# Optimization experiments

Measured on AMD Instinct MI355X. Metric: run time of the kernel, lower is better.

Reference implementation:

```python
import jax, jax.numpy as jnp
import numpy as np

SR = 22050
FL = 1024      # window_samples
FP = 256       # step_samples
FCEIL = 10000  # formant ceiling (Hz)
MAXF = 4       # max formants
AP_ORDER = 10
R_ORDER = 30
FMIN, FMAX = 50, 500
DK_ITERS = 60  # Durand-Kerner iterations (replaces companion-matrix eig; differentiable)

_w = np.blackman(FL)
WIN = jnp.asarray(_w / np.sqrt(np.sum(_w ** 2)), jnp.float32)  # power-normalized blackman (diffsptk default)


def _frame(x):
    # center-padded framing, frames = T//FP + 1
    pad = FL // 2
    xp = jnp.pad(x, ((0, 0), (pad, pad)))
    n_frames = x.shape[-1] // FP + 1
    idx = jnp.arange(n_frames)[:, None] * FP + jnp.arange(FL)[None, :]
    return xp[:, idx]  # [B, F, FL]


def _levinson(r, order):
    # Levinson-Durbin on autocorrelation r[..., :order+1].
    # Returns (allpole poly coeffs a[..., order+1] with a0=1, reflection coeffs k[..., order]).
    a = jnp.zeros(r.shape[:-1] + (order + 1,), r.dtype).at[..., 0].set(1.0)
    E = r[..., 0]
    ks = []
    for m in range(1, order + 1):
        if m == 1:
            acc = r[..., 1]
        else:
            acc = r[..., m] + jnp.sum(a[..., 1:m] * r[..., m - 1:0:-1], axis=-1)
        k = -acc / (E + 1e-9)
        a_prev = a
        a = a.at[..., m].set(k)
        if m > 1:
            a = a.at[..., 1:m].add(k[..., None] * a_prev[..., m - 1:0:-1])
        E = E * (1.0 - k * k)
        ks.append(k)
    return a, jnp.stack(ks, axis=-1)


def _poly_roots(coeffs):
    # Durand-Kerner simultaneous root iteration, vectorized over frames.
    n = coeffs.shape[-1] - 1
    c = (coeffs / coeffs[..., :1]).astype(jnp.complex64)
    z0 = (0.4 + 0.9j) ** jnp.arange(1, n + 1)
    z = jnp.broadcast_to(z0, c.shape[:-1] + (n,)).astype(jnp.complex64)
    eye = jnp.eye(n, dtype=jnp.complex64)
    def step(z, _):
        p = jnp.zeros_like(z)
        for i in range(n + 1):  # Horner eval of poly at all current root estimates
            p = p * z + c[..., i:i + 1]
        diff = z[..., :, None] - z[..., None, :] + eye
        z = z - p / (jnp.prod(diff, axis=-1) + 1e-12)
        return z, None
    z, _ = jax.lax.scan(step, z, None, length=DK_ITERS)
    return z  # [..., n]


def _root_to_formant(roots):
    # downsampled spectrum covers 0..FCEIL/2, so freq = angle/(2*pi)*FCEIL
    ang = jnp.angle(roots)
    freq = ang / (2.0 * jnp.pi) * FCEIL
    freq = jnp.where(ang > 1e-4, freq, FCEIL * 0.5)  # keep upper-half-plane roots only
    return jnp.sort(freq, axis=-1)[..., :MAXF]  # [B, F, MAXF]


def _pitch(x):
    # autocorrelation pitch tracker
    xf = _frame(x)
    spec = jnp.fft.rfft(xf)
    ac = jnp.fft.irfft(spec * jnp.conj(spec))
    lag_min, lag_max = SR // FMAX, SR // FMIN  # 44..441
    seg = ac[..., lag_min:lag_max + 1]
    peak = jnp.max(seg, axis=-1)
    idx = jnp.argmax(seg, axis=-1)
    nccf = peak / (ac[..., 0] + 1e-9)
    pitch = SR / (lag_min + idx).astype(jnp.float32)
    voicing = (nccf > 0.3).astype(jnp.float32)
    return pitch, voicing, nccf


def _forward(x):
    xf = _frame(x)                 # [B, F, FL]
    xw = xf * WIN
    spec = jnp.fft.rfft(xw)        # [B, F, 513]
    nb = spec.shape[-1]
    ds = int(FCEIL / SR * nb)      # 232 bins -> Nyquist FCEIL/2
    x_ds = spec[..., :ds]
    ac_ds = jnp.fft.irfft(x_ds * jnp.conj(x_ds))   # [B, F, 462]
    ac_us = jnp.fft.irfft(spec * jnp.conj(spec))   # [B, F, 1024]
    ap_env, _ = _levinson(ac_ds, AP_ORDER)
    _, r_coeff_ref = _levinson(ac_us, R_ORDER)
    roots = _poly_roots(ap_env)
    formants = _root_to_formant(roots)
    energy = 10.0 * jnp.log10(jnp.sum(xf * xf, axis=-1) + 1e-10)
    mag = jnp.abs(jnp.fft.rfft(xf))
    freqs = jnp.arange(nb, dtype=jnp.float32) * (SR / FL)
    centroid = jnp.sum(mag * freqs, axis=-1) / (jnp.sum(mag, axis=-1) + 1e-10)
    tilt = ac_ds[..., 1] / (ac_ds[..., 0] + 1e-10)
    pitch, voicing, nccf = _pitch(x)
    pitch = jnp.log(pitch)
    return (formants, energy, centroid, tilt, pitch, voicing, r_coeff_ref, x_ds, nccf)


def setup_inputs() -> dict:
    key = jax.random.key(0)
    x = jax.random.normal(key, (8, 661500), jnp.float32)
    return {"x": x}


def reference(x):
    return _forward(x)
```

## Files before the change

### kernel.cpp

```cpp
#include <hip/hip_runtime.h>
#include <math.h>

#define NSAMP   661500
#define NFRAME  2584
#define NFTOT   20672

#define EN_OFF    82688
#define CEN_OFF   103360
#define TILT_OFF  124032
#define PITCH_OFF 144704
#define VOI_OFF   165376
#define RC_OFF    186048
#define XDS_OFF   806208

__device__ __forceinline__ float waveReduceSum(float v) {
  #pragma unroll
  for (int m = 1; m < 64; m <<= 1) v += __shfl_xor(v, m, 64);
  return v;
}

__device__ __forceinline__ float blockReduceSum(float v, float* s) {
  v = waveReduceSum(v);
  const int w = threadIdx.x >> 6;
  if ((threadIdx.x & 63) == 0) s[w] = v;
  __syncthreads();
  v = s[0] + s[1] + s[2] + s[3];
  __syncthreads();
  return v;
}

__device__ __forceinline__ void blockReduceSum2(float& v0, float& v1, float* s) {
  v0 = waveReduceSum(v0);
  v1 = waveReduceSum(v1);
  const int w = threadIdx.x >> 6;
  if ((threadIdx.x & 63) == 0) { s[w] = v0; s[4 + w] = v1; }
  __syncthreads();
  v0 = s[0] + s[1] + s[2] + s[3];
  v1 = s[4] + s[5] + s[6] + s[7];
  __syncthreads();
}

__device__ __forceinline__ void fft1024p(float2* X, float2* Y, const float2* tw, int tid) {
  int m = 1;
  #pragma unroll
  for (int s = 0; s < 5; ++s) {
    const int k  = tid & (m - 1);
    const int jm = tid - k;
    const float2 a0 = X[tid];
    const float2 a1 = X[tid + 256];
    const float2 a2 = X[tid + 512];
    const float2 a3 = X[tid + 768];
    const float2 w1 = tw[jm];
    float2 sA, dA, sB, dB;
    sA.x = a0.x + a2.x; sA.y = a0.y + a2.y;
    { const float dx = a0.x - a2.x, dy = a0.y - a2.y;
      dA.x = dx * w1.x + dy * w1.y;
      dA.y = dy * w1.x - dx * w1.y; }
    sB.x = a1.x + a3.x; sB.y = a1.y + a3.y;
    { const float dx = a1.x - a3.x, dy = a1.y - a3.y;
      const float wx = -w1.y, wy = w1.x;
      dB.x = dx * wx + dy * wy;
      dB.y = dy * wx - dx * wy; }
    const float w2x = w1.x * w1.x - w1.y * w1.y;
    const float w2y = 2.0f * w1.x * w1.y;
    const int B = 4 * tid - 3 * k;
    { float2 o;
      o.x = sA.x + sB.x; o.y = sA.y + sB.y;
      Y[B] = o;
      const float dx = sA.x - sB.x, dy = sA.y - sB.y;
      o.x = dx * w2x + dy * w2y;
      o.y = dy * w2x - dx * w2y;
      Y[B + 2 * m] = o; }
    { float2 o;
      o.x = dA.x + dB.x; o.y = dA.y + dB.y;
      Y[B + m] = o;
      const float dx = dA.x - dB.x, dy = dA.y - dB.y;
      o.x = dx * w2x + dy * w2y;
      o.y = dy * w2x - dx * w2y;
      Y[B + 3 * m] = o; }
    __syncthreads();
    float2* tmp = X; X = Y; Y = tmp;
    m <<= 2;
  }
}

template<int ORDER>
__device__ __forceinline__ void levinson_d(const double* r, double* a) {
  double E = r[0];
  a[0] = 1.0;
  #pragma unroll
  for (int m = 1; m <= ORDER; ++m) {
    double acc = r[m];
    #pragma unroll
    for (int i = 1; i < m; ++i) acc += a[i] * r[m - i];
    const double kk = -acc / (E + 1e-9);
    #pragma unroll
    for (int i = 1; i <= (m - 1) / 2; ++i) {
      const double t1 = a[i], t2 = a[m - i];
      a[i]     = t1 + kk * t2;
      a[m - i] = t2 + kk * t1;
    }
    if ((m & 1) == 0) { const double t = a[m >> 1]; a[m >> 1] = t + kk * t; }
    a[m] = kk;
    E *= (1.0 - kk * kk);
  }
}

__device__ __forceinline__ void levinson_f30(const float* r, float* gk) {
  float a[31];
  float E = r[0];
  a[0] = 1.0f;
  #pragma unroll
  for (int m = 1; m <= 30; ++m) {
    float acc = r[m];
    #pragma unroll
    for (int i = 1; i < m; ++i) acc += a[i] * r[m - i];
    const float kk = -acc / (E + 1e-9f);
    #pragma unroll
    for (int i = 1; i <= (m - 1) / 2; ++i) {
      const float t1 = a[i], t2 = a[m - i];
      a[i]     = t1 + kk * t2;
      a[m - i] = t2 + kk * t1;
    }
    if ((m & 1) == 0) { const float t = a[m >> 1]; a[m >> 1] = t + kk * t; }
    a[m] = kk;
    E *= (1.0f - kk * kk);
    if (gk) gk[m - 1] = kk;
  }
}

__global__ void __launch_bounds__(256, 6)
feat_mono4(const float* __restrict__ x, float* __restrict__ out,
           const int xds_pf, const int nccf_off) {
  __shared__ float2 A[1024];
  __shared__ float2 Bb[1024];
  __shared__ float2 tw[256];
  __shared__ float  Pw[232];
  __shared__ float  sred[8];
  __shared__ int    sredi[4];
  __shared__ float  stash[4][42];
  __shared__ float  aprt[4][11];

  const int tid   = threadIdx.x;
  const int w     = tid >> 6;
  const int lane  = tid & 63;
  const int fbase = blockIdx.x * 4;

  {
    const float th = (float)tid * (6.2831853071795864769f / 1024.0f);
    float sn, cn;
    sincosf(th, &sn, &cn);
    tw[tid] = make_float2(cn, sn);
  }
  float wv[4];
  float wsq = 0.0f;
  #pragma unroll
  for (int q = 0; q < 4; ++q) {
    const int n = tid + q * 256;
    const float th = (float)n * (6.2831853071795864769f / 1023.0f);
    const float wn = 0.42f - 0.5f * cosf(th) + 0.08f * cosf(2.0f * th);
    wv[q] = wn;
    wsq += wn * wn;
  }
  float ctab[11];
  #pragma unroll
  for (int l = 0; l < 11; ++l)
    ctab[l] = cosf((float)(tid * l) * (6.2831853071795864769f / 462.0f));
  const float wgt462 = ((tid == 0 || tid == 231) ? 1.0f : 2.0f) * (1.0f / 462.0f);
  __syncthreads();
  const float invn = 1.0f / sqrtf(blockReduceSum(wsq, sred));

  #pragma unroll 1
  for (int p = 0; p < 4; ++p) {
    const int fg = fbase + p;
    const int bb = fg / NFRAME;
    const int fr = fg - bb * NFRAME;
    const float* xb = x + (size_t)bb * NSAMP;

    float esum = 0.0f;
    #pragma unroll
    for (int q = 0; q < 4; ++q) {
      const int n = tid + q * 256;
      const int g = fr * 256 + n - 512;
      const float xv = (g >= 0 && g < NSAMP) ? xb[g] : 0.0f;
      esum += xv * xv;
      A[n] = make_float2(xv * wv[q] * invn, xv);
    }
    esum = waveReduceSum(esum);
    if (lane == 0) sred[w] = esum;
    __syncthreads();
    if (tid == 0) {
      const float en = sred[0] + sred[1] + sred[2] + sred[3];
      out[EN_OFF + fg] = 10.0f * log10f(en + 1e-10f);
    }

    fft1024p(A, Bb, tw, tid);

    float cs0 = 0.0f, cs1 = 0.0f;
    for (int k = tid; k < 513; k += 256) {
      const float2 Zk = Bb[k];
      const float2 Zn = Bb[(1024 - k) & 1023];
      const float xwr = 0.5f * (Zk.x + Zn.x);
      const float xwi = 0.5f * (Zk.y - Zn.y);
      const float xfr = 0.5f * (Zk.y + Zn.y);
      const float xfi = -0.5f * (Zk.x - Zn.x);
      const float pw = xwr * xwr + xwi * xwi;
      const float pf = xfr * xfr + xfi * xfi;
      const float mg = sqrtf(pf);
      cs0 += mg;
      cs1 += mg * ((float)k * (22050.0f / 1024.0f));
      if (k < 232) {
        Pw[k] = pw;
        if (xds_pf == 232) {
          out[XDS_OFF + (size_t)fg * 232 + k] = xwr;
        } else {
          out[XDS_OFF + (size_t)fg * 464 + 2 * k]     = xwr;
          out[XDS_OFF + (size_t)fg * 464 + 2 * k + 1] = xwi;
        }
      }
    }
    blockReduceSum2(cs0, cs1, sred);
    if (tid == 0) out[CEN_OFF + fg] = cs1 / (cs0 + 1e-10f);

    #pragma unroll
    for (int q = 0; q < 4; ++q) {
      const int k2 = tid + q * 256;
      const int km = (k2 <= 512) ? k2 : (1024 - k2);
      const float2 Zk = Bb[km];
      const float2 Zn = Bb[(1024 - km) & 1023];
      const float xwr = 0.5f * (Zk.x + Zn.x);
      const float xwi = 0.5f * (Zk.y - Zn.y);
      const float xfr = 0.5f * (Zk.y + Zn.y);
      const float xfi = -0.5f * (Zk.x - Zn.x);
      const float pw = xwr * xwr + xwi * xwi;
      const float pf = xfr * xfr + xfi * xfi;
      A[k2] = make_float2(pw * 1024.0f, pf);
    }
    __syncthreads();

    fft1024p(A, Bb, tw, tid);

    float pv = -3.0e38f;
    int   pl = 1 << 30;
    for (int l = 44 + tid; l <= 441; l += 256) {
      const float v = Bb[l].y;
      if (v > pv) { pv = v; pl = l; }
    }
    #pragma unroll
    for (int m = 1; m < 64; m <<= 1) {
      const float ov = __shfl_xor(pv, m, 64);
      const int   ol = __shfl_xor(pl, m, 64);
      if (ov > pv || (ov == pv && ol < pl)) { pv = ov; pl = ol; }
    }
    if (lane == 0) { sred[w] = pv; sredi[w] = pl; }
    __syncthreads();
    if (tid == 0) {
      float bv = sred[0]; int bl = sredi[0];
      #pragma unroll
      for (int q = 1; q < 4; ++q)
        if (sred[q] > bv || (sred[q] == bv && sredi[q] < bl)) { bv = sred[q]; bl = sredi[q]; }
      const float ac0  = Bb[0].y * (1.0f / 1024.0f);
      const float peak = bv * (1.0f / 1024.0f);
      const float nccf = peak / (ac0 + 1e-9f);
      out[PITCH_OFF + fg] = logf(22050.0f / (float)bl);
      out[VOI_OFF + fg]   = (nccf > 0.3f) ? 1.0f : 0.0f;
      out[nccf_off + fg]  = nccf;
    }

    const float pwW = (tid < 232) ? Pw[tid] * wgt462 : 0.0f;
    #pragma unroll
    for (int l = 0; l < 11; ++l) {
      const float t = waveReduceSum(pwW * ctab[l]);
      if (lane == 0) aprt[w][l] = t;
    }
    __syncthreads();
    if (tid < 11)
      stash[p][31 + tid] = aprt[0][tid] + aprt[1][tid] + aprt[2][tid] + aprt[3][tid];
    if (tid == 0) {
      const float a0 = aprt[0][0] + aprt[1][0] + aprt[2][0] + aprt[3][0];
      const float a1 = aprt[0][1] + aprt[1][1] + aprt[2][1] + aprt[3][1];
      out[TILT_OFF + fg] = a1 / (a0 + 1e-10f);
    }
    if (tid < 31) stash[p][tid] = Bb[tid].x * (1.0f / 1048576.0f);
    __syncthreads();
  }

  if (w == 0) {
    const int g     = lane >> 4;
    const int ri    = lane & 15;
    const int gbase = g << 4;
    const int fg    = fbase + g;

    levinson_f30(&stash[g][0],
                 (ri == 0) ? (out + RC_OFF + (size_t)fg * 30) : (float*)nullptr);

    double rds[11], a10[11];
    #pragma unroll
    for (int l = 0; l < 11; ++l) rds[l] = (double)stash[g][31 + l];
    levinson_d<10>(rds, a10);

    double zr = 0.4, zi = 0.9;
    for (int q = 0; q < ri; ++q) {
      const double nr = zr * 0.4 - zi * 0.9;
      zi = zr * 0.9 + zi * 0.4;
      zr = nr;
    }
    for (int it = 0; it < 60; ++it) {
      double pr = 1.0, pi = 0.0;
      #pragma unroll
      for (int q = 1; q <= 10; ++q) {
        const double nr = pr * zr - pi * zi + a10[q];
        pi = pr * zi + pi * zr;
        pr = nr;
      }
      double dr = 1.0, di = 0.0;
      #pragma unroll
      for (int j = 0; j < 10; ++j) {
        const double ozr = __shfl(zr, gbase + j, 64);
        const double ozi = __shfl(zi, gbase + j, 64);
        const double er = (j == ri) ? 1.0 : (zr - ozr);
        const double ei = (j == ri) ? 0.0 : (zi - ozi);
        const double nr = dr * er - di * ei;
        di = dr * ei + di * er;
        dr = nr;
      }
      dr += 1e-12;
      const double d2 = dr * dr + di * di;
      const double qr = (pr * dr + pi * di) / d2;
      const double qi = (pi * dr - pr * di) / d2;
      zr -= qr;
      zi -= qi;
    }
    const double ang = atan2(zi, zr);
    double freq = (ang > 0.0001) ? (ang / 6.283185307179586476925287 * 10000.0) : 5000.0;
    if (ri >= 10) freq = 1.0e300;
    double fsel[4];
    #pragma unroll
    for (int p2 = 0; p2 < 4; ++p2) {
      double mn = freq;
      #pragma unroll
      for (int m = 1; m < 16; m <<= 1) mn = fmin(mn, __shfl_xor(mn, m, 64));
      fsel[p2] = mn;
      const unsigned long long bal =
          __ballot(freq == mn) & (0xFFFFULL << gbase);
      const int low = (int)__builtin_ctzll(bal);
      if (lane == low) freq = 1.0e300;
    }
    if (ri == 0) {
      out[(size_t)fg * 4 + 0] = (float)fsel[0];
      out[(size_t)fg * 4 + 1] = (float)fsel[1];
      out[(size_t)fg * 4 + 2] = (float)fsel[2];
      out[(size_t)fg * 4 + 3] = (float)fsel[3];
    }
  }
}

extern "C" void kernel_launch(void* const* d_in, const int* in_sizes, int n_in,
                              void* d_out, int out_size, void* d_ws, size_t ws_size,
                              hipStream_t stream) {
  (void)in_sizes; (void)n_in; (void)d_ws; (void)ws_size;
  const float* x = (const float*)d_in[0];
  float* out = (float*)d_out;
  int xds_pf = 232;
  if (out_size >= XDS_OFF + NFTOT * 464 + NFTOT) xds_pf = 464;
  const int nccf_off = XDS_OFF + NFTOT * xds_pf;
  feat_mono4<<<dim3(NFTOT / 4), dim3(256), 0, stream>>>(x, out, xds_pf, nccf_off);
}
```

Before: 379.1 us.

## Process six frames per block and pack root-finding lanes ten per frame

Each block now handles six frames instead of four, and the wave-0 Durand-Kerner stage packs ten lanes per frame instead of sixteen, so 60 of 64 lanes do useful work. This cuts the per-block setup cost (twiddles, window, cos table) and the serial root-finding tail relative to the frame work. The formant top-4 selection becomes a per-lane sort over shuffled values rather than ballot-based reductions, and the complex division uses one reciprocal. Launch bounds are raised to 7 blocks per SM, which may force register spilling. The last block handles a partial tile, which adds guard logic.

```diff
diff --git a/kernel.cpp b/kernel.cpp
--- a/kernel.cpp
+++ b/kernel.cpp
@@ -4,6 +4,8 @@
 #define NSAMP   661500
 #define NFRAME  2584
 #define NFTOT   20672
+#define FPB     6
+#define NBLK    3446
 
 #define EN_OFF    82688
 #define CEN_OFF   103360
@@ -129,8 +131,8 @@
   }
 }
 
-__global__ void __launch_bounds__(256, 6)
-feat_mono4(const float* __restrict__ x, float* __restrict__ out,
+__global__ void __launch_bounds__(256, 7)
+feat_mono6(const float* __restrict__ x, float* __restrict__ out,
            const int xds_pf, const int nccf_off) {
   __shared__ float2 A[1024];
   __shared__ float2 Bb[1024];
@@ -138,13 +140,14 @@
   __shared__ float  Pw[232];
   __shared__ float  sred[8];
   __shared__ int    sredi[4];
-  __shared__ float  stash[4][42];
+  __shared__ float  stash[FPB][42];
   __shared__ float  aprt[4][11];
 
   const int tid   = threadIdx.x;
   const int w     = tid >> 6;
   const int lane  = tid & 63;
-  const int fbase = blockIdx.x * 4;
+  const int fbase = blockIdx.x * FPB;
+  const int np    = (fbase + FPB <= NFTOT) ? FPB : (NFTOT - fbase);
 
   {
     const float th = (float)tid * (6.2831853071795864769f / 1024.0f);
@@ -171,7 +174,7 @@
   const float invn = 1.0f / sqrtf(blockReduceSum(wsq, sred));
 
   #pragma unroll 1
-  for (int p = 0; p < 4; ++p) {
+  for (int p = 0; p < np; ++p) {
     const int fg = fbase + p;
     const int bb = fg / NFRAME;
     const int fr = fg - bb * NFRAME;
@@ -286,17 +289,19 @@
   }
 
   if (w == 0) {
-    const int g     = lane >> 4;
-    const int ri    = lane & 15;
-    const int gbase = g << 4;
-    const int fg    = fbase + g;
-
-    levinson_f30(&stash[g][0],
-                 (ri == 0) ? (out + RC_OFF + (size_t)fg * 30) : (float*)nullptr);
+    const int g     = lane / 10;
+    const int ri    = lane - g * 10;
+    const int gbase = g * 10;
+    const int gg    = (g < FPB) ? g : (FPB - 1);
+    const bool act  = (g < np);
+    const int fg    = fbase + gg;
+
+    levinson_f30(&stash[gg][0],
+                 (ri == 0 && act) ? (out + RC_OFF + (size_t)fg * 30) : (float*)nullptr);
 
     double rds[11], a10[11];
     #pragma unroll
-    for (int l = 0; l < 11; ++l) rds[l] = (double)stash[g][31 + l];
+    for (int l = 0; l < 11; ++l) rds[l] = (double)stash[gg][31 + l];
     levinson_d<10>(rds, a10);
 
     double zr = 0.4, zi = 0.9;
@@ -325,32 +330,38 @@
         dr = nr;
       }
       dr += 1e-12;
-      const double d2 = dr * dr + di * di;
-      const double qr = (pr * dr + pi * di) / d2;
-      const double qi = (pi * dr - pr * di) / d2;
+      const double inv = 1.0 / (dr * dr + di * di);
+      const double qr = (pr * dr + pi * di) * inv;
+      const double qi = (pi * dr - pr * di) * inv;
       zr -= qr;
       zi -= qi;
     }
     const double ang = atan2(zi, zr);
     double freq = (ang > 0.0001) ? (ang / 6.283185307179586476925287 * 10000.0) : 5000.0;
     if (ri >= 10) freq = 1.0e300;
-    double fsel[4];
+
+    double f[10];
+    #pragma unroll
+    for (int j = 0; j < 10; ++j) f[j] = __shfl(freq, gbase + j, 64);
+    bool used[10];
+    #pragma unroll
+    for (int j = 0; j < 10; ++j) used[j] = false;
+    float o4[4];
     #pragma unroll
     for (int p2 = 0; p2 < 4; ++p2) {
-      double mn = freq;
+      double mn = 1.0e300;
+      int mj = -1;
       #pragma unroll
-      for (int m = 1; m < 16; m <<= 1) mn = fmin(mn, __shfl_xor(mn, m, 64));
-      fsel[p2] = mn;
-      const unsigned long long bal =
-          __ballot(freq == mn) & (0xFFFFULL << gbase);
-      const int low = (int)__builtin_ctzll(bal);
-      if (lane == low) freq = 1.0e300;
-    }
-    if (ri == 0) {
-      out[(size_t)fg * 4 + 0] = (float)fsel[0];
-      out[(size_t)fg * 4 + 1] = (float)fsel[1];
-      out[(size_t)fg * 4 + 2] = (float)fsel[2];
-      out[(size_t)fg * 4 + 3] = (float)fsel[3];
+      for (int j = 0; j < 10; ++j)
+        if (!used[j] && f[j] < mn) { mn = f[j]; mj = j; }
+      if (mj >= 0) used[mj] = true;
+      o4[p2] = (float)mn;
+    }
+    if (ri == 0 && act) {
+      out[(size_t)fg * 4 + 0] = o4[0];
+      out[(size_t)fg * 4 + 1] = o4[1];
+      out[(size_t)fg * 4 + 2] = o4[2];
+      out[(size_t)fg * 4 + 3] = o4[3];
     }
   }
 }
@@ -364,5 +375,5 @@
   int xds_pf = 232;
   if (out_size >= XDS_OFF + NFTOT * 464 + NFTOT) xds_pf = 464;
   const int nccf_off = XDS_OFF + NFTOT * xds_pf;
-  feat_mono4<<<dim3(NFTOT / 4), dim3(256), 0, stream>>>(x, out, xds_pf, nccf_off);
-}
+  feat_mono6<<<dim3(NBLK), dim3(256), 0, stream>>>(x, out, xds_pf, nccf_off);
+}
```

Result: faster. 337.4 us (-11.0%).
